# Kernel tuning notes

Measured on AMD Instinct MI355X. Metric: run time of the kernel, lower is better.

## Reference

```python
import jax, jax.numpy as jnp
import numpy as np

N, C, R = 8192, 512, 8
DK = C // R  # 64

def setup_inputs() -> dict:
    key = jax.random.key(0)
    k1, k2, kq, kk, kv = jax.random.split(key, 5)
    s = 0.05
    return {
        "im1": jax.random.normal(k1, (N, C), jnp.float32),
        "im2": jax.random.normal(k2, (N, C), jnp.float32),
        "Wq": jax.random.normal(kq, (C, DK), jnp.float32) * s,
        "Wk": jax.random.normal(kk, (C, DK), jnp.float32) * s,
        "Wv": jax.random.normal(kv, (C, C), jnp.float32) * s,
    }

def reference(im1, im2, Wq, Wk, Wv):
    # shared projections (weights stored as [in, out]; torch Linear is x @ W.T)
    im1_q = im1 @ Wq  # [N, DK]
    im1_k = im1 @ Wk  # [N, DK]
    im1_v = im1 @ Wv  # [N, C]
    im2_q = im2 @ Wq
    im2_k = im2 @ Wk
    im2_v = im2 @ Wv
    # cross attention (no scaling in original)
    im1_attn = jax.nn.softmax(im2_q @ im1_k.T, axis=-1)  # [N, N]
    im2_attn = jax.nn.softmax(im1_q @ im2_k.T, axis=-1)  # [N, N]
    im1_out = im1_attn @ im1_v + im1
    im2_out = im2_attn @ im2_v + im2
    return im1_out, im2_out
```

## Files before the change

### kernel.cpp

```cpp
#include <hip/hip_runtime.h>

#define NN 8192
#define CC 512
#define DKK 64

typedef float f32x4 __attribute__((ext_vector_type(4)));
typedef float f32x16 __attribute__((ext_vector_type(16)));
typedef _Float16 f16x8 __attribute__((ext_vector_type(8)));
typedef _Float16 f16x4 __attribute__((ext_vector_type(4)));

__device__ __forceinline__ f32x4 mfma16(f16x8 a, f16x8 b, f32x4 c) {
    return __builtin_amdgcn_mfma_f32_16x16x32_f16(a, b, c, 0, 0, 0);
}
__device__ __forceinline__ f32x16 mfma32(f16x8 a, f16x8 b, f32x16 c) {
    return __builtin_amdgcn_mfma_f32_32x32x16_f16(a, b, c, 0, 0, 0);
}
__device__ __forceinline__ f16x8 sclh8(f16x8 v, _Float16 h) {
    f16x8 r;
#pragma unroll
    for (int i = 0; i < 8; i++) r[i] = v[i] * h;
    return r;
}
__device__ __forceinline__ float exp2fast(float x) { return __builtin_exp2f(x); }

__global__ void wtrans_all_kernel(const float* __restrict__ Wq, const float* __restrict__ Wk,
                                  const float* __restrict__ Wv,
                                  _Float16* __restrict__ Wqt, _Float16* __restrict__ Wkt,
                                  _Float16* __restrict__ Wvf) {
    int idx = blockIdx.x * 256 + threadIdx.x;
    if (idx < 32768) {
        int n = idx >> 9, k = idx & 511;
        Wqt[idx] = (_Float16)Wq[k * 64 + n];
    } else if (idx < 65536) {
        int j = idx - 32768;
        int n = j >> 9, k = j & 511;
        Wkt[j] = (_Float16)Wk[k * 64 + n];
    } else {
        int j = idx - 65536;
        int k16 = j & 15, c = (j >> 4) & 511, ks = j >> 13;
        Wvf[j] = (_Float16)Wv[(size_t)(16 * ks + k16) * 512 + c];
    }
}

__global__ __launch_bounds__(256) void proj_qk2_kernel(
    const float* __restrict__ im1, const float* __restrict__ im2,
    const _Float16* __restrict__ Wqt, const _Float16* __restrict__ Wkt,
    _Float16* __restrict__ Q1, _Float16* __restrict__ Kf1,
    _Float16* __restrict__ Q2, _Float16* __restrict__ Kf2)
{
    const float* X = blockIdx.y ? im2 : im1;
    _Float16* Q = blockIdx.y ? Q2 : Q1;
    _Float16* Kf = blockIdx.y ? Kf2 : Kf1;

    __shared__ __align__(16) _Float16 Wlds[128 * 512];

    const int tid = threadIdx.x;
    const int lane = tid & 63, wave = tid >> 6;
    const int n16 = lane & 15, quad = lane >> 4;

#pragma unroll
    for (int i = 0; i < 32; i++) {
        const int idx = tid + 256 * i;
        const int row = idx >> 6, ch = idx & 63;
        const _Float16* src = (row < 64) ? (Wqt + (size_t)row * 512 + ch * 8)
                                         : (Wkt + (size_t)(row - 64) * 512 + ch * 8);
        *(f16x8*)&Wlds[row * 512 + ((ch ^ (row & 7)) * 8)] = *(const f16x8*)src;
    }
    __syncthreads();

    const int arow = blockIdx.x * 64 + wave * 16 + n16;
    f32x4 acc[8];
#pragma unroll
    for (int i = 0; i < 8; i++) acc[i] = (f32x4){0.f, 0.f, 0.f, 0.f};

    const float* xbase = X + (size_t)arow * 512 + quad * 8;
    for (int kk = 0; kk < 16; kk++) {
        f32x4 xa = *(const f32x4*)(xbase + kk * 32);
        f32x4 xb = *(const f32x4*)(xbase + kk * 32 + 4);
        f16x8 afrag;
#pragma unroll
        for (int j = 0; j < 4; j++) { afrag[j] = (_Float16)xa[j]; afrag[4 + j] = (_Float16)xb[j]; }
#pragma unroll
        for (int t = 0; t < 8; t++) {
            const int row = t * 16 + n16;
            f16x8 bfr = *(const f16x8*)&Wlds[row * 512 + (((4 * kk + quad) ^ (row & 7)) * 8)];
            acc[t] = mfma16(afrag, bfr, acc[t]);
        }
    }
    const int rbase = blockIdx.x * 64 + wave * 16 + quad * 4;
#pragma unroll
    for (int t = 0; t < 4; t++)
#pragma unroll
        for (int r = 0; r < 4; r++) {
            Q[(size_t)(rbase + r) * 64 + t * 16 + n16] = (_Float16)(acc[t][r] * 1.44269504f);
            Kf[((size_t)(blockIdx.x * 4 + t) * 64 + (wave * 16 + quad * 4 + r)) * 16 + n16] =
                (_Float16)acc[4 + t][r];
        }
}

__global__ __launch_bounds__(256) void proj_vt_kernel(
    const float* __restrict__ im1, const float* __restrict__ im2,
    const _Float16* __restrict__ Wvf,
    _Float16* __restrict__ Vf1, _Float16* __restrict__ Vf2)
{
    const float* X = blockIdx.y ? im2 : im1;
    _Float16* Vf = blockIdx.y ? Vf2 : Vf1;
    const int n0 = blockIdx.x * 32;
    const int tid = threadIdx.x;
    const int lane = tid & 63, wave = tid >> 6;
    const int l31 = lane & 31, lhi = lane >> 5;

    __shared__ __align__(16) _Float16 Xlds[32 * 512];

#pragma unroll
    for (int i = 0; i < 8; i++) {
        const int n = tid >> 3;
        const int chunk = (tid & 7) + 8 * i;
        const float* xp = X + (size_t)(n0 + n) * CC + chunk * 8;
        f32x4 x0 = *(const f32x4*)xp;
        f32x4 x1 = *(const f32x4*)(xp + 4);
        f16x8 d;
#pragma unroll
        for (int j = 0; j < 4; j++) { d[j] = (_Float16)x0[j]; d[4 + j] = (_Float16)x1[j]; }
        *(f16x8*)&Xlds[n * 512 + ((chunk ^ (n & 7)) * 8)] = d;
    }
    __syncthreads();

    f32x16 acc[4];
#pragma unroll
    for (int t = 0; t < 4; t++)
#pragma unroll
        for (int r = 0; r < 16; r++) acc[t][r] = 0.f;

    for (int ks = 0; ks < 32; ks++) {
        f16x8 xb = *(const f16x8*)&Xlds[l31 * 512 + (((2 * ks + lhi) ^ (l31 & 7)) * 8)];
#pragma unroll
        for (int ct = 0; ct < 4; ct++) {
            const _Float16* wp = Wvf + ((size_t)ks * 512 + 128 * wave + 32 * ct + l31) * 16 + 8 * lhi;
            acc[ct] = mfma32(*(const f16x8*)wp, xb, acc[ct]);
        }
    }
    const int tile = n0 >> 6;
    const int ksbase = (n0 & 32) >> 4;
#pragma unroll
    for (int ct = 0; ct < 4; ct++)
#pragma unroll
        for (int r = 0; r < 16; r++) {
            const int c = 128 * wave + 32 * ct + (r & 3) + 8 * (r >> 2) + 4 * lhi;
            const int ks = ksbase + (l31 >> 4);
            Vf[((size_t)(tile * 4 + ks) * 512 + c) * 16 + (l31 & 15)] = (_Float16)acc[ct][r];
        }
}

__global__ __launch_bounds__(1024, 4) void flash17_kernel(
    const _Float16* __restrict__ Q1, const _Float16* __restrict__ Kf1,
    const _Float16* __restrict__ Q2, const _Float16* __restrict__ Kf2,
    const _Float16* __restrict__ Vf1, const _Float16* __restrict__ Vf2,
    const float* __restrict__ im1, const float* __restrict__ im2,
    float* __restrict__ out)
{
    const int bid = blockIdx.x;
    const int img = bid & 1;
    const int qbase = (bid >> 1) * 64;
    const _Float16* Q = img ? Q1 : Q2;
    const _Float16* Kf = img ? Kf2 : Kf1;
    const _Float16* Vf = img ? Vf2 : Vf1;
    const float* res = img ? im2 : im1;
    float* o = out + (size_t)img * NN * CC;

    __shared__ __align__(16) _Float16 Vs[2][4 * 512 * 16];
    __shared__ __align__(16) _Float16 P[2][8][64][8];
    __shared__ float mPart[2][2][64];
    __shared__ float mF[2][64], lF[2][64];

    const int tid = threadIdx.x;
    const int lane = tid & 63, w = tid >> 6;
    const int l31 = lane & 31, lhi = lane >> 5;
    const bool isqk = (w < 4);
    const int a = w & 1, b = (w >> 1) & 1;

    f32x16 acc[2];
#pragma unroll
    for (int t = 0; t < 2; t++)
#pragma unroll
        for (int r = 0; r < 16; r++) acc[t][r] = 0.f;
    float mg_run[2] = {-3e38f, -3e38f};

    f16x8 qf[4], kreg[4];
    float ma_run = -3e38f, l_run = 0.f;

    const _Float16* kb = Kf + (size_t)(32 * a + l31) * 16 + 8 * lhi;

    if (isqk) {
        const _Float16* qp = Q + (size_t)(qbase + 32 * b + l31) * DKK + 8 * lhi;
#pragma unroll
        for (int k = 0; k < 4; k++) qf[k] = *(const f16x8*)(qp + 16 * k);
#pragma unroll
        for (int k = 0; k < 4; k++) kreg[k] = *(const f16x8*)(kb + (size_t)k * 1024);
    }

    f16x8 st0, st1, st2, st3;
    auto stage_issue = [&](int t) {
        const _Float16* src = Vf + (size_t)t * 32768 + w * 2048 + lane * 8;
        st0 = *(const f16x8*)(src);
        st1 = *(const f16x8*)(src + 512);
        st2 = *(const f16x8*)(src + 1024);
        st3 = *(const f16x8*)(src + 1536);
    };
    auto stage_write = [&](int t) {
        _Float16* dst = &Vs[t & 1][0] + w * 2048 + lane * 8;
        *(f16x8*)(dst) = st0;
        *(f16x8*)(dst + 512) = st1;
        *(f16x8*)(dst + 1024) = st2;
        *(f16x8*)(dst + 1536) = st3;
    };

    auto do_qk = [&](int tt) {
        const int pbuf = tt & 1;
        f32x16 sA;
#pragma unroll
        for (int r = 0; r < 16; r++) sA[r] = 0.f;
#pragma unroll
        for (int k = 0; k < 4; k++) sA = mfma32(kreg[k], qf[k], sA);
        if (tt + 1 < 128) {
#pragma unroll
            for (int k = 0; k < 4; k++)
                kreg[k] = *(const f16x8*)(kb + (size_t)((tt + 1) * 4 + k) * 1024);
        }
        float mr[8];
#pragma unroll
        for (int i = 0; i < 8; i++) mr[i] = fmaxf(sA[i], sA[i + 8]);
#pragma unroll
        for (int i = 0; i < 4; i++) mr[i] = fmaxf(mr[i], mr[i + 4]);
        float mx = fmaxf(fmaxf(mr[0], mr[1]), fmaxf(mr[2], mr[3]));
        mx = fmaxf(mx, __shfl_xor(mx, 32));
        const float manew = fmaxf(ma_run, mx);
        if (lane < 32) mPart[pbuf][a][32 * b + lane] = manew;
        float ls = 0.f;
#pragma unroll
        for (int r = 0; r < 16; r++) {
            float p = exp2fast(sA[r] - manew);
            ls += p;
            sA[r] = p;
        }
        ls += __shfl_xor(ls, 32);
        l_run = l_run * exp2fast(ma_run - manew) + ls;
        ma_run = manew;
#pragma unroll
        for (int gg = 0; gg < 4; gg++) {
            f16x4 p4;
#pragma unroll
            for (int u = 0; u < 4; u++) p4[u] = (_Float16)sA[gg * 4 + u];
            *(f16x4*)&P[pbuf][4 * a + gg][32 * b + l31][4 * lhi] = p4;
        }
    };

    stage_issue(0);
    if (isqk) do_qk(0);
    stage_write(0);
    __syncthreads();

    for (int s = 0; s < 128; s++) {
        const int pbuf = s & 1;
        if (s < 127) {
            stage_issue(s + 1);
            if (isqk) do_qk(s + 1);
        }

        float f[2][2], al[2];
#pragma unroll
        for (int qh = 0; qh < 2; qh++) {
            float mgn = mg_run[qh];
#pragma unroll
            for (int a2 = 0; a2 < 2; a2++) {
                f[qh][a2] = mPart[pbuf][a2][32 * qh + l31];
                mgn = fmaxf(mgn, f[qh][a2]);
            }
            al[qh] = exp2fast(mg_run[qh] - mgn);
            mg_run[qh] = mgn;
#pragma unroll
            for (int a2 = 0; a2 < 2; a2++) f[qh][a2] = exp2fast(f[qh][a2] - mgn);
        }
        if (!__all((al[0] == 1.f) & (al[1] == 1.f))) {
#pragma unroll
            for (int qh = 0; qh < 2; qh++)
#pragma unroll
                for (int r = 0; r < 16; r++) acc[qh][r] *= al[qh];
        }

        const _Float16* vbufp = &Vs[pbuf][0];
#pragma unroll
        for (int ks = 0; ks < 4; ks++) {
            f16x8 va = *(const f16x8*)(vbufp + ks * 8192 + (32 * w + l31) * 16 + 8 * lhi);
            f16x8 pb0 = *(const f16x8*)&P[pbuf][2 * ks + lhi][l31][0];
            f16x8 pb1 = *(const f16x8*)&P[pbuf][2 * ks + lhi][32 + l31][0];
            pb0 = sclh8(pb0, (_Float16)f[0][ks >> 1]);
            pb1 = sclh8(pb1, (_Float16)f[1][ks >> 1]);
            acc[0] = mfma32(va, pb0, acc[0]);
            acc[1] = mfma32(va, pb1, acc[1]);
        }

        if (s < 127) stage_write(s + 1);
        __syncthreads();
    }

    if (isqk && lane < 32) {
        mF[a][32 * b + lane] = ma_run;
        lF[a][32 * b + lane] = l_run;
    }
    __syncthreads();

    float fac[2];
#pragma unroll
    for (int qh = 0; qh < 2; qh++) {
        const int q = 32 * qh + l31;
        const float M = mg_run[qh];
        float den = 0.f;
#pragma unroll
        for (int a2 = 0; a2 < 2; a2++)
            den += lF[a2][q] * exp2fast(mF[a2][q] - M);
        fac[qh] = 1.f / den;
    }

#pragma unroll
    for (int qh = 0; qh < 2; qh++)
#pragma unroll
        for (int rg = 0; rg < 4; rg++) {
            const int c = 32 * w + 8 * rg + 4 * lhi;
            const size_t off = (size_t)(qbase + 32 * qh + l31) * CC + c;
            f32x4 v;
#pragma unroll
            for (int u = 0; u < 4; u++) v[u] = acc[qh][4 * rg + u] * fac[qh];
            f32x4 r4 = *(const f32x4*)(res + off);
            *(f32x4*)(o + off) = v + r4;
        }
}

extern "C" void kernel_launch(void* const* d_in, const int* in_sizes, int n_in,
                              void* d_out, int out_size, void* d_ws, size_t ws_size,
                              hipStream_t stream) {
    const float* im1 = (const float*)d_in[0];
    const float* im2 = (const float*)d_in[1];
    const float* Wq  = (const float*)d_in[2];
    const float* Wk  = (const float*)d_in[3];
    const float* Wv  = (const float*)d_in[4];
    float* out = (float*)d_out;

    _Float16* w = (_Float16*)d_ws;
    _Float16* Wqt = w;
    _Float16* Wkt = Wqt + 64 * 512;
    _Float16* Wvf = Wkt + 64 * 512;
    _Float16* Q1  = Wvf + 512 * 512;
    _Float16* Kf1 = Q1 + NN * DKK;
    _Float16* Q2  = Kf1 + NN * DKK;
    _Float16* Kf2 = Q2 + NN * DKK;
    _Float16* Vf1 = Kf2 + NN * DKK;
    _Float16* Vf2 = Vf1 + (size_t)CC * NN;

    wtrans_all_kernel<<<1280, 256, 0, stream>>>(Wq, Wk, Wv, Wqt, Wkt, Wvf);
    proj_qk2_kernel<<<dim3(128, 2), 256, 0, stream>>>(im1, im2, Wqt, Wkt, Q1, Kf1, Q2, Kf2);
    proj_vt_kernel<<<dim3(256, 2), 256, 0, stream>>>(im1, im2, Wvf, Vf1, Vf2);
    flash17_kernel<<<256, 1024, 0, stream>>>(Q1, Kf1, Q2, Kf2, Vf1, Vf2, im1, im2, out);
}
```

Before: 388.7 us.

## Split V tile layout into k-halves, spread QK waves, add no-rescale fast path

The V projection now writes each 16-wide key block as two separate 8-wide halves, so the flash kernel's shared-memory reads of V become contiguous 8-element rows. This is meant to reduce LDS bank conflicts. The four QK/softmax waves move from waves 0-3 to waves 0,5,10,15, which spreads the extra softmax work across SIMDs. QK waves now seed their running max with the global max, so partial maxima more often equal it, and a wave-uniform fast path skips the exp2 rescaling and the P scaling when no max changed. The cost is duplicated MFMA loop code and a branch on every step.

```diff
diff --git a/kernel.cpp b/kernel.cpp
--- a/kernel.cpp
+++ b/kernel.cpp
@@ -148,11 +148,13 @@
         for (int r = 0; r < 16; r++) {
             const int c = 128 * wave + 32 * ct + (r & 3) + 8 * (r >> 2) + 4 * lhi;
             const int ks = ksbase + (l31 >> 4);
-            Vf[((size_t)(tile * 4 + ks) * 512 + c) * 16 + (l31 & 15)] = (_Float16)acc[ct][r];
-        }
-}
-
-__global__ __launch_bounds__(1024, 4) void flash17_kernel(
+            const int k16 = l31 & 15;
+            Vf[(size_t)(tile * 4 + ks) * 8192 + (k16 >> 3) * 4096 + c * 8 + (k16 & 7)] =
+                (_Float16)acc[ct][r];
+        }
+}
+
+__global__ __launch_bounds__(1024, 4) void flash18_kernel(
     const _Float16* __restrict__ Q1, const _Float16* __restrict__ Kf1,
     const _Float16* __restrict__ Q2, const _Float16* __restrict__ Kf2,
     const _Float16* __restrict__ Vf1, const _Float16* __restrict__ Vf2,
@@ -168,7 +170,7 @@
     const float* res = img ? im2 : im1;
     float* o = out + (size_t)img * NN * CC;
 
-    __shared__ __align__(16) _Float16 Vs[2][4 * 512 * 16];
+    __shared__ __align__(16) _Float16 Vs[2][4 * 2 * 512 * 8];
     __shared__ __align__(16) _Float16 P[2][8][64][8];
     __shared__ float mPart[2][2][64];
     __shared__ float mF[2][64], lF[2][64];
@@ -176,8 +178,9 @@
     const int tid = threadIdx.x;
     const int lane = tid & 63, w = tid >> 6;
     const int l31 = lane & 31, lhi = lane >> 5;
-    const bool isqk = (w < 4);
-    const int a = w & 1, b = (w >> 1) & 1;
+    const bool isqk = (w == 0) | (w == 5) | (w == 10) | (w == 15);
+    const int qi = w / 5;
+    const int a = qi & 1, b = qi >> 1;
 
     f32x16 acc[2];
 #pragma unroll
@@ -215,17 +218,17 @@
         *(f16x8*)(dst + 1536) = st3;
     };
 
-    auto do_qk = [&](int tt) {
-        const int pbuf = tt & 1;
+    auto do_qk = [&](int ss) {
+        const int pbuf = ss & 1;
         f32x16 sA;
 #pragma unroll
         for (int r = 0; r < 16; r++) sA[r] = 0.f;
 #pragma unroll
         for (int k = 0; k < 4; k++) sA = mfma32(kreg[k], qf[k], sA);
-        if (tt + 1 < 128) {
+        if (ss + 1 < 128) {
 #pragma unroll
             for (int k = 0; k < 4; k++)
-                kreg[k] = *(const f16x8*)(kb + (size_t)((tt + 1) * 4 + k) * 1024);
+                kreg[k] = *(const f16x8*)(kb + (size_t)((ss + 1) * 4 + k) * 1024);
         }
         float mr[8];
 #pragma unroll
@@ -234,7 +237,7 @@
         for (int i = 0; i < 4; i++) mr[i] = fmaxf(mr[i], mr[i + 4]);
         float mx = fmaxf(fmaxf(mr[0], mr[1]), fmaxf(mr[2], mr[3]));
         mx = fmaxf(mx, __shfl_xor(mx, 32));
-        const float manew = fmaxf(ma_run, mx);
+        const float manew = fmaxf(fmaxf(mg_run[b], ma_run), mx);
         if (lane < 32) mPart[pbuf][a][32 * b + lane] = manew;
         float ls = 0.f;
 #pragma unroll
@@ -267,37 +270,55 @@
             if (isqk) do_qk(s + 1);
         }
 
-        float f[2][2], al[2];
+        float lal[2], lf0[2], lf1[2];
+        bool fastall = true;
 #pragma unroll
         for (int qh = 0; qh < 2; qh++) {
-            float mgn = mg_run[qh];
-#pragma unroll
-            for (int a2 = 0; a2 < 2; a2++) {
-                f[qh][a2] = mPart[pbuf][a2][32 * qh + l31];
-                mgn = fmaxf(mgn, f[qh][a2]);
+            const int q = 32 * qh + l31;
+            const float m0 = mPart[pbuf][0][q];
+            const float m1 = mPart[pbuf][1][q];
+            const float mgo = mg_run[qh];
+            const float mgn = fmaxf(mgo, fmaxf(m0, m1));
+            fastall &= (m0 == mgn) & (m1 == mgn) & (mgo == mgn);
+            mg_run[qh] = mgn;
+            lal[qh] = mgo - mgn;
+            lf0[qh] = m0 - mgn;
+            lf1[qh] = m1 - mgn;
+        }
+        const bool nos = __all(fastall);
+        const _Float16* vbufp = &Vs[pbuf][0];
+
+        if (nos) {
+#pragma unroll
+            for (int ks = 0; ks < 4; ks++) {
+                f16x8 va = *(const f16x8*)(vbufp + (ks * 2 + lhi) * 4096 + (32 * w + l31) * 8);
+                f16x8 pb0 = *(const f16x8*)&P[pbuf][2 * ks + lhi][l31][0];
+                f16x8 pb1 = *(const f16x8*)&P[pbuf][2 * ks + lhi][32 + l31][0];
+                acc[0] = mfma32(va, pb0, acc[0]);
+                acc[1] = mfma32(va, pb1, acc[1]);
             }
-            al[qh] = exp2fast(mg_run[qh] - mgn);
-            mg_run[qh] = mgn;
-#pragma unroll
-            for (int a2 = 0; a2 < 2; a2++) f[qh][a2] = exp2fast(f[qh][a2] - mgn);
-        }
-        if (!__all((al[0] == 1.f) & (al[1] == 1.f))) {
+        } else {
+            float f[2][2], al[2];
+#pragma unroll
+            for (int qh = 0; qh < 2; qh++) {
+                al[qh] = exp2fast(lal[qh]);
+                f[qh][0] = exp2fast(lf0[qh]);
+                f[qh][1] = exp2fast(lf1[qh]);
+            }
 #pragma unroll
             for (int qh = 0; qh < 2; qh++)
 #pragma unroll
                 for (int r = 0; r < 16; r++) acc[qh][r] *= al[qh];
-        }
-
-        const _Float16* vbufp = &Vs[pbuf][0];
-#pragma unroll
-        for (int ks = 0; ks < 4; ks++) {
-            f16x8 va = *(const f16x8*)(vbufp + ks * 8192 + (32 * w + l31) * 16 + 8 * lhi);
-            f16x8 pb0 = *(const f16x8*)&P[pbuf][2 * ks + lhi][l31][0];
-            f16x8 pb1 = *(const f16x8*)&P[pbuf][2 * ks + lhi][32 + l31][0];
-            pb0 = sclh8(pb0, (_Float16)f[0][ks >> 1]);
-            pb1 = sclh8(pb1, (_Float16)f[1][ks >> 1]);
-            acc[0] = mfma32(va, pb0, acc[0]);
-            acc[1] = mfma32(va, pb1, acc[1]);
+#pragma unroll
+            for (int ks = 0; ks < 4; ks++) {
+                f16x8 va = *(const f16x8*)(vbufp + (ks * 2 + lhi) * 4096 + (32 * w + l31) * 8);
+                f16x8 pb0 = *(const f16x8*)&P[pbuf][2 * ks + lhi][l31][0];
+                f16x8 pb1 = *(const f16x8*)&P[pbuf][2 * ks + lhi][32 + l31][0];
+                pb0 = sclh8(pb0, (_Float16)f[0][ks >> 1]);
+                pb1 = sclh8(pb1, (_Float16)f[1][ks >> 1]);
+                acc[0] = mfma32(va, pb0, acc[0]);
+                acc[1] = mfma32(va, pb1, acc[1]);
+            }
         }
 
         if (s < 127) stage_write(s + 1);
@@ -360,5 +381,5 @@
     wtrans_all_kernel<<<1280, 256, 0, stream>>>(Wq, Wk, Wv, Wqt, Wkt, Wvf);
     proj_qk2_kernel<<<dim3(128, 2), 256, 0, stream>>>(im1, im2, Wqt, Wkt, Q1, Kf1, Q2, Kf2);
     proj_vt_kernel<<<dim3(256, 2), 256, 0, stream>>>(im1, im2, Wvf, Vf1, Vf2);
-    flash17_kernel<<<256, 1024, 0, stream>>>(Q1, Kf1, Q2, Kf2, Vf1, Vf2, im1, im2, out);
-}
+    flash18_kernel<<<256, 1024, 0, stream>>>(Q1, Kf1, Q2, Kf2, Vf1, Vf2, im1, im2, out);
+}
```

New measurement: 1.344 ms. +245.8%, slower.
